# Optimization experiments

Measured on AMD Instinct MI355X. Metric: run time of the kernel, lower is better.

The kernel has to match this reference:

```python
import jax, jax.numpy as jnp
import numpy as np

B = 2097152  # number of Gaussians


def setup_inputs() -> dict:
    key = jax.random.key(0)
    k1, k2, k3, k4, k5, k6 = jax.random.split(key, 6)
    return {
        "loc1": jax.random.normal(k1, (B, 3), dtype=jnp.float32),
        "scale1": jax.random.uniform(k2, (B, 3), dtype=jnp.float32),
        "rot_matrix1": jax.random.normal(k3, (B, 3, 3), dtype=jnp.float32),
        "loc2": jax.random.normal(k4, (B, 3), dtype=jnp.float32),
        "scale2": jax.random.uniform(k5, (B, 3), dtype=jnp.float32),
        "rot_matrix2": jax.random.normal(k6, (B, 3, 3), dtype=jnp.float32),
    }


def reference(loc1, scale1, rot_matrix1, loc2, scale2, rot_matrix2):
    # ||mu1 - mu2||^2  -> (B,)
    loc_diff2 = jnp.sum((loc1 - loc2) ** 2, axis=-1)

    # cov2 = R2 diag(scale2) R2^T  -> (B,3,3)
    cov2 = jnp.einsum("bij,bj,bkj->bik", rot_matrix2, scale2, rot_matrix2)
    # cov2 rotated into frame of Gaussian 1: R1^T cov2 R1  -> (B,3,3)
    cov2_R1 = jnp.einsum("bji,bjk,bkl->bil", rot_matrix1, cov2, rot_matrix1)

    # E = diag(sqrt(s1)) cov2_R1 diag(sqrt(s1)), then symmetrize
    s1_sqrt = jnp.sqrt(scale1)  # (B,3)
    E = s1_sqrt[:, :, None] * cov2_R1 * s1_sqrt[:, None, :]
    E = (E + jnp.swapaxes(E, 1, 2)) * 0.5

    # trace of matrix sqrt via eigenvalues: sum (lambda^2)^(1/4) = sum |lambda|^(1/2)
    E_eig = jnp.linalg.eigvalsh(E)  # (B,3)
    E_sqrt_trace = jnp.sum(jnp.sqrt(jnp.sqrt(E_eig ** 2)), axis=-1)

    cov_wasserstein = jnp.sum(scale1, axis=-1) + jnp.sum(scale2, axis=-1) - 2.0 * E_sqrt_trace
    cov_wasserstein = jnp.maximum(cov_wasserstein, 0.0)
    return jnp.sqrt(loc_diff2 + cov_wasserstein)
```

## Files before the change

### kernel.cpp

```cpp
#include <hip/hip_runtime.h>
#include <math.h>

#define BLK 256

struct Elem {
    float l1[3], l2[3], s1[3], s2[3], R1[9], R2[9];
};

__device__ __forceinline__ void load_elem(
    const float* __restrict__ loc1, const float* __restrict__ scale1,
    const float* __restrict__ rot1, const float* __restrict__ loc2,
    const float* __restrict__ scale2, const float* __restrict__ rot2,
    int idx, Elem& e)
{
    __builtin_memcpy(e.R1, rot1   + (size_t)idx * 9, 36);
    __builtin_memcpy(e.R2, rot2   + (size_t)idx * 9, 36);
    __builtin_memcpy(e.l1, loc1   + (size_t)idx * 3, 12);
    __builtin_memcpy(e.l2, loc2   + (size_t)idx * 3, 12);
    __builtin_memcpy(e.s1, scale1 + (size_t)idx * 3, 12);
    __builtin_memcpy(e.s2, scale2 + (size_t)idx * 3, 12);
}

__device__ __forceinline__ float compute(const Elem& e)
{
    const float dx = e.l1[0] - e.l2[0];
    const float dy = e.l1[1] - e.l2[1];
    const float dz = e.l1[2] - e.l2[2];
    const float ld2 = dx * dx + dy * dy + dz * dz;

    const float* R1 = e.R1;
    const float* R2 = e.R2;
    const float sa = e.s1[0], sb = e.s1[1], sc = e.s1[2];
    const float ua = e.s2[0], ub = e.s2[1], uc = e.s2[2];

    const float m00 = ua * R2[0] * R2[0] + ub * R2[1] * R2[1] + uc * R2[2] * R2[2];
    const float m01 = ua * R2[0] * R2[3] + ub * R2[1] * R2[4] + uc * R2[2] * R2[5];
    const float m02 = ua * R2[0] * R2[6] + ub * R2[1] * R2[7] + uc * R2[2] * R2[8];
    const float m11 = ua * R2[3] * R2[3] + ub * R2[4] * R2[4] + uc * R2[5] * R2[5];
    const float m12 = ua * R2[3] * R2[6] + ub * R2[4] * R2[7] + uc * R2[5] * R2[8];
    const float m22 = ua * R2[6] * R2[6] + ub * R2[7] * R2[7] + uc * R2[8] * R2[8];

    const float A0 = m00 * R1[0] + m01 * R1[3] + m02 * R1[6];
    const float A1 = m00 * R1[1] + m01 * R1[4] + m02 * R1[7];
    const float A2 = m00 * R1[2] + m01 * R1[5] + m02 * R1[8];
    const float A3 = m01 * R1[0] + m11 * R1[3] + m12 * R1[6];
    const float A4 = m01 * R1[1] + m11 * R1[4] + m12 * R1[7];
    const float A5 = m01 * R1[2] + m11 * R1[5] + m12 * R1[8];
    const float A6 = m02 * R1[0] + m12 * R1[3] + m22 * R1[6];
    const float A7 = m02 * R1[1] + m12 * R1[4] + m22 * R1[7];
    const float A8 = m02 * R1[2] + m12 * R1[5] + m22 * R1[8];

    const float t00 = R1[0] * A0 + R1[3] * A3 + R1[6] * A6;
    const float t01 = R1[0] * A1 + R1[3] * A4 + R1[6] * A7;
    const float t02 = R1[0] * A2 + R1[3] * A5 + R1[6] * A8;
    const float t11 = R1[1] * A1 + R1[4] * A4 + R1[7] * A7;
    const float t12 = R1[1] * A2 + R1[4] * A5 + R1[7] * A8;
    const float t22 = R1[2] * A2 + R1[5] * A5 + R1[8] * A8;

    const float c2 = t00 * sa + t11 * sb + t22 * sc;
    const float g2 = t00 * t00 * sa * sa + t11 * t11 * sb * sb + t22 * t22 * sc * sc
                   + 2.0f * (t01 * t01 * sa * sb + t02 * t02 * sa * sc + t12 * t12 * sb * sc);
    const float c1 = 0.5f * (c2 * c2 - g2);
    const float detT = t00 * (t11 * t22 - t12 * t12)
                     - t01 * (t01 * t22 - t12 * t02)
                     + t02 * (t01 * t12 - t11 * t02);
    const float c0 = detT * sa * sb * sc;

    const float m  = c2 * (1.0f / 3.0f);
    const float p  = c1 - c2 * m;
    const float q  = c1 * m - 2.0f * m * m * m - c0;
    const float s  = __builtin_amdgcn_sqrtf(fmaxf(-p * (1.0f / 3.0f), 0.0f));
    const float s3 = 2.0f * s * s * s;
    const float inv = __builtin_amdgcn_rcpf(fmaxf(s3, 1e-30f));
    float u = -q * inv;
    u = fminf(fmaxf(u, -1.0f), 1.0f);

    const float au = fabsf(u);
    const float rr = __builtin_amdgcn_sqrtf(1.0f - au) *
        (1.5707288f + au * (-0.2121144f + au * (0.0742610f + au * (-0.0187293f))));
    const float ac = (u < 0.0f) ? (3.14159265358979f - rr) : rr;

    const float phi = ac * (1.0f / (3.0f * 6.283185307179586f));
    const float x0 = 2.0f * s * __builtin_amdgcn_cosf(phi);
    const float x1 = 2.0f * s * __builtin_amdgcn_cosf(phi - (1.0f / 3.0f));
    const float e0 = x0 + m;
    const float e1 = x1 + m;
    const float e2 = c2 - e0 - e1;

    const float tr = __builtin_amdgcn_sqrtf(fabsf(e0))
                   + __builtin_amdgcn_sqrtf(fabsf(e1))
                   + __builtin_amdgcn_sqrtf(fabsf(e2));

    float cw = (sa + sb + sc) + (ua + ub + uc) - 2.0f * tr;
    cw = fmaxf(cw, 0.0f);
    return __builtin_amdgcn_sqrtf(ld2 + cw);
}

__global__ __launch_bounds__(BLK, 4) void wasserstein_kernel(
    const float* __restrict__ loc1,   const float* __restrict__ scale1,
    const float* __restrict__ rot1,   const float* __restrict__ loc2,
    const float* __restrict__ scale2, const float* __restrict__ rot2,
    float* __restrict__ out, int S)
{
    const int t = blockIdx.x * BLK + threadIdx.x;

    Elem a, b;
    load_elem(loc1, scale1, rot1, loc2, scale2, rot2, t, a);
    load_elem(loc1, scale1, rot1, loc2, scale2, rot2, t + S, b);

    const float r0 = compute(a);
    load_elem(loc1, scale1, rot1, loc2, scale2, rot2, t + 2 * S, a);
    out[t] = r0;

    const float r1 = compute(b);
    load_elem(loc1, scale1, rot1, loc2, scale2, rot2, t + 3 * S, b);
    out[t + S] = r1;

    out[t + 2 * S] = compute(a);
    out[t + 3 * S] = compute(b);
}

extern "C" void kernel_launch(void* const* d_in, const int* in_sizes, int n_in,
                              void* d_out, int out_size, void* d_ws, size_t ws_size,
                              hipStream_t stream) {
    const float* loc1   = (const float*)d_in[0];
    const float* scale1 = (const float*)d_in[1];
    const float* rot1   = (const float*)d_in[2];
    const float* loc2   = (const float*)d_in[3];
    const float* scale2 = (const float*)d_in[4];
    const float* rot2   = (const float*)d_in[5];
    float* out = (float*)d_out;

    const int B = in_sizes[0] / 3;
    const int S = B / 4;
    const int grid = S / BLK;

    wasserstein_kernel<<<grid, BLK, 0, stream>>>(loc1, scale1, rot1,
                                                 loc2, scale2, rot2, out, S);
}
```

Measured before the change: 241.6 us.

## Process four contiguous elements per thread with 16-byte nontemporal vector loads

Each thread now handles four adjacent Gaussians instead of four strided ones. That makes its input slices 16-byte aligned, so all inputs are fetched with float4 nontemporal loads and the four results are written with a single float4 nontemporal store. The aim is to replace many misaligned 12- and 36-byte scalar loads with wide vector transactions. The cost is more live registers (about 120 input floats per thread), so launch bounds are lowered to 3 waves, and adjacent lanes now touch addresses 48 or 144 bytes apart, which may weaken coalescing.

```diff
diff --git a/kernel.cpp b/kernel.cpp
--- a/kernel.cpp
+++ b/kernel.cpp
@@ -3,35 +3,25 @@
 
 #define BLK 256
 
-struct Elem {
-    float l1[3], l2[3], s1[3], s2[3], R1[9], R2[9];
-};
+typedef float vfloat4 __attribute__((ext_vector_type(4)));
 
-__device__ __forceinline__ void load_elem(
-    const float* __restrict__ loc1, const float* __restrict__ scale1,
-    const float* __restrict__ rot1, const float* __restrict__ loc2,
-    const float* __restrict__ scale2, const float* __restrict__ rot2,
-    int idx, Elem& e)
-{
-    __builtin_memcpy(e.R1, rot1   + (size_t)idx * 9, 36);
-    __builtin_memcpy(e.R2, rot2   + (size_t)idx * 9, 36);
-    __builtin_memcpy(e.l1, loc1   + (size_t)idx * 3, 12);
-    __builtin_memcpy(e.l2, loc2   + (size_t)idx * 3, 12);
-    __builtin_memcpy(e.s1, scale1 + (size_t)idx * 3, 12);
-    __builtin_memcpy(e.s2, scale2 + (size_t)idx * 3, 12);
+__device__ __forceinline__ void nt_load4(float* dst, const float* __restrict__ src) {
+    const vfloat4 v = __builtin_nontemporal_load(reinterpret_cast<const vfloat4*>(src));
+    dst[0] = v.x; dst[1] = v.y; dst[2] = v.z; dst[3] = v.w;
 }
 
-__device__ __forceinline__ float compute(const Elem& e)
+__device__ __forceinline__ float compute(
+    const float* R1, const float* R2,
+    const float* l1, const float* l2,
+    const float* s1, const float* s2)
 {
-    const float dx = e.l1[0] - e.l2[0];
-    const float dy = e.l1[1] - e.l2[1];
-    const float dz = e.l1[2] - e.l2[2];
+    const float dx = l1[0] - l2[0];
+    const float dy = l1[1] - l2[1];
+    const float dz = l1[2] - l2[2];
     const float ld2 = dx * dx + dy * dy + dz * dz;
 
-    const float* R1 = e.R1;
-    const float* R2 = e.R2;
-    const float sa = e.s1[0], sb = e.s1[1], sc = e.s1[2];
-    const float ua = e.s2[0], ub = e.s2[1], uc = e.s2[2];
+    const float sa = s1[0], sb = s1[1], sc = s1[2];
+    const float ua = s2[0], ub = s2[1], uc = s2[2];
 
     const float m00 = ua * R2[0] * R2[0] + ub * R2[1] * R2[1] + uc * R2[2] * R2[2];
     const float m01 = ua * R2[0] * R2[3] + ub * R2[1] * R2[4] + uc * R2[2] * R2[5];
@@ -96,28 +86,41 @@
     return __builtin_amdgcn_sqrtf(ld2 + cw);
 }
 
-__global__ __launch_bounds__(BLK, 4) void wasserstein_kernel(
+__global__ __launch_bounds__(BLK, 3) void wasserstein_kernel(
     const float* __restrict__ loc1,   const float* __restrict__ scale1,
     const float* __restrict__ rot1,   const float* __restrict__ loc2,
     const float* __restrict__ scale2, const float* __restrict__ rot2,
-    float* __restrict__ out, int S)
+    float* __restrict__ out)
 {
     const int t = blockIdx.x * BLK + threadIdx.x;
+    const int g = t * 4;
 
-    Elem a, b;
-    load_elem(loc1, scale1, rot1, loc2, scale2, rot2, t, a);
-    load_elem(loc1, scale1, rot1, loc2, scale2, rot2, t + S, b);
+    float r1[36], r2[36], l1[12], l2[12], s1[12], s2[12];
 
-    const float r0 = compute(a);
-    load_elem(loc1, scale1, rot1, loc2, scale2, rot2, t + 2 * S, a);
-    out[t] = r0;
+#pragma unroll
+    for (int i = 0; i < 9; ++i) nt_load4(r1 + i * 4, rot1 + (size_t)g * 9 + i * 4);
+#pragma unroll
+    for (int i = 0; i < 9; ++i) nt_load4(r2 + i * 4, rot2 + (size_t)g * 9 + i * 4);
+#pragma unroll
+    for (int i = 0; i < 3; ++i) nt_load4(l1 + i * 4, loc1 + (size_t)g * 3 + i * 4);
+#pragma unroll
+    for (int i = 0; i < 3; ++i) nt_load4(l2 + i * 4, loc2 + (size_t)g * 3 + i * 4);
+#pragma unroll
+    for (int i = 0; i < 3; ++i) nt_load4(s1 + i * 4, scale1 + (size_t)g * 3 + i * 4);
+#pragma unroll
+    for (int i = 0; i < 3; ++i) nt_load4(s2 + i * 4, scale2 + (size_t)g * 3 + i * 4);
 
-    const float r1 = compute(b);
-    load_elem(loc1, scale1, rot1, loc2, scale2, rot2, t + 3 * S, b);
-    out[t + S] = r1;
+    float res[4];
+#pragma unroll
+    for (int j = 0; j < 4; ++j) {
+        res[j] = compute(r1 + 9 * j, r2 + 9 * j,
+                         l1 + 3 * j, l2 + 3 * j,
+                         s1 + 3 * j, s2 + 3 * j);
+    }
 
-    out[t + 2 * S] = compute(a);
-    out[t + 3 * S] = compute(b);
+    vfloat4 o;
+    o.x = res[0]; o.y = res[1]; o.z = res[2]; o.w = res[3];
+    __builtin_nontemporal_store(o, reinterpret_cast<vfloat4*>(out + g));
 }
 
 extern "C" void kernel_launch(void* const* d_in, const int* in_sizes, int n_in,
@@ -132,9 +135,8 @@
     float* out = (float*)d_out;
 
     const int B = in_sizes[0] / 3;
-    const int S = B / 4;
-    const int grid = S / BLK;
+    const int grid = B / (4 * BLK);
 
     wasserstein_kernel<<<grid, BLK, 0, stream>>>(loc1, scale1, rot1,
-                                                 loc2, scale2, rot2, out, S);
+                                                 loc2, scale2, rot2, out);
 }
```

Measured after the change: 326.0 us. 1.35x slower.
